# Performance work log

Measured on AMD Instinct MI355X. Metric: run time of the kernel, lower is better.

The kernel has to match this reference:

```python
import jax, jax.numpy as jnp
import numpy as np

H = 1024
NH = 16
HD = H // NH

def setup_inputs() -> dict:
    key = jax.random.key(0)
    ks = jax.random.split(key, 8)
    s = 1.0 / np.sqrt(H)
    hidden_states = jax.random.normal(ks[0], (2, 2048, H), dtype=jnp.float32)
    attention_mask = jnp.zeros((2, 1, 1, 2048), dtype=jnp.float32)
    Wq = jax.random.uniform(ks[1], (H, H), jnp.float32, -s, s)
    bq = jax.random.uniform(ks[2], (H,), jnp.float32, -s, s)
    Wk = jax.random.uniform(ks[3], (H, H), jnp.float32, -s, s)
    bk = jax.random.uniform(ks[4], (H,), jnp.float32, -s, s)
    Wv = jax.random.uniform(ks[5], (H, H), jnp.float32, -s, s)
    bv = jax.random.uniform(ks[6], (H,), jnp.float32, -s, s)
    return {"hidden_states": hidden_states, "attention_mask": attention_mask,
            "Wq": Wq, "bq": bq, "Wk": Wk, "bk": bk, "Wv": Wv, "bv": bv}

def _split_heads(x):
    B, L, _ = x.shape
    return x.reshape(B, L, NH, HD).transpose(0, 2, 1, 3)  # [B, nh, L, hd]

def reference(hidden_states, attention_mask, Wq, bq, Wk, bk, Wv, bv):
    # QKV projections (nn.Linear: x @ W.T + b)
    Q = _split_heads(hidden_states @ Wq.T + bq)
    K = _split_heads(hidden_states @ Wk.T + bk)
    V = _split_heads(hidden_states @ Wv.T + bv)
    scale = 1.0 / np.sqrt(HD)
    scores = jnp.einsum('bhqd,bhkd->bhqk', Q, K) * scale  # [B, nh, L, L]
    scores = scores + attention_mask
    probs = jax.nn.softmax(scores, axis=-1)  # dropout in eval mode = identity
    context = jnp.einsum('bhqk,bhkd->bhqd', probs, V)
    B, _, L, _ = context.shape
    return context.transpose(0, 2, 1, 3).reshape(B, L, H)
```

## Files before the change

kernel.cpp:

```cpp
#include <hip/hip_runtime.h>
#include <math.h>
#include <stdint.h>

#define H_DIM 1024
#define NH 16
#define HD 64
#define B_DIM 2
#define L_DIM 2048
#define M_TOT (B_DIM * L_DIM)

typedef __bf16 bf16_t;
typedef __bf16 bf16x8 __attribute__((ext_vector_type(8)));
typedef __bf16 bf16x4 __attribute__((ext_vector_type(4)));
typedef float  f32x4  __attribute__((ext_vector_type(4)));

#define AS1 const __attribute__((address_space(1))) void*
#define AS3 __attribute__((address_space(3))) void*

__global__ __launch_bounds__(256)
void cast_all(const float* __restrict__ x,
              const float* __restrict__ Wq, const float* __restrict__ Wk,
              const float* __restrict__ Wv, bf16_t* __restrict__ dst)
{
    const size_t idx = ((size_t)blockIdx.x * 256 + threadIdx.x) * 4;
    const float* src;
    size_t off;
    if (idx < (size_t)M_TOT * H_DIM) { src = x; off = idx; }
    else {
        size_t j = idx - (size_t)M_TOT * H_DIM;
        int z = (int)(j >> 20);
        off = j & ((1u << 20) - 1);
        src = (z == 0) ? Wq : (z == 1) ? Wk : Wv;
    }
    const float4 v = *(const float4*)(src + off);
    bf16x4 o;
    o[0] = (bf16_t)v.x; o[1] = (bf16_t)v.y;
    o[2] = (bf16_t)v.z; o[3] = (bf16_t)v.w;
    *(bf16x4*)(dst + idx) = o;
}

__global__ __launch_bounds__(256, 2)
void qkv_mfma(const bf16_t* __restrict__ xb, const bf16_t* __restrict__ wb,
              const float* __restrict__ bq, const float* __restrict__ bk,
              const float* __restrict__ bv,
              bf16_t* __restrict__ qb, bf16_t* __restrict__ kb,
              bf16_t* __restrict__ vt)
{
    __shared__ bf16_t As0[128 * 32];
    __shared__ bf16_t As1[128 * 32];
    __shared__ bf16_t As2[128 * 32];
    __shared__ bf16_t Bs0[3][64 * 32];
    __shared__ bf16_t Bs1[3][64 * 32];
    __shared__ bf16_t Bs2[3][64 * 32];

    const int tid = threadIdx.x;
    const int n   = blockIdx.x;
    const int m8  = n >> 3;
    const int bn  = ((n & 7) * 2 + (m8 & 1)) * 64;
    const int bm  = (m8 >> 1) * 128;

    const int wave = tid >> 6;
    const int lane = tid & 63;
    const int lc   = lane & 15;
    const int quad = lane >> 4;

    f32x4 acc[3][2][4];
    #pragma unroll
    for (int z = 0; z < 3; ++z)
        #pragma unroll
        for (int i = 0; i < 2; ++i)
            #pragma unroll
            for (int j = 0; j < 4; ++j)
                acc[z][i][j] = (f32x4){0.f, 0.f, 0.f, 0.f};

    const int srow = tid >> 2;
    const int sseg = tid & 3;
    const bf16_t* gA = xb + (size_t)(bm + srow) * H_DIM + (sseg ^ (srow & 3)) * 8;
    const bf16_t* gB = wb + (size_t)(bn + srow) * H_DIM + (sseg ^ (srow & 3)) * 8;
    const int woff = wave * 1024;

    auto stage = [&](int k0, bf16_t* A_, bf16_t (*B_)[64 * 32]) {
        __builtin_amdgcn_global_load_lds((AS1)(gA + k0),
            (AS3)((char*)A_ + woff), 16, 0, 0);
        __builtin_amdgcn_global_load_lds((AS1)(gA + k0 + (size_t)64 * H_DIM),
            (AS3)((char*)A_ + woff + 4096), 16, 0, 0);
        #pragma unroll
        for (int z = 0; z < 3; ++z)
            __builtin_amdgcn_global_load_lds(
                (AS1)(gB + (size_t)z * H_DIM * H_DIM + k0),
                (AS3)((char*)B_[z] + woff), 16, 0, 0);
    };

    const int slot = (quad ^ (lc & 3)) * 8;
    auto compute = [&](const bf16_t* A_, const bf16_t (*B_)[64 * 32]) {
        bf16x8 a[2];
        #pragma unroll
        for (int mi = 0; mi < 2; ++mi)
            a[mi] = *(const bf16x8*)(A_ + (wave * 32 + mi * 16 + lc) * 32 + slot);
        #pragma unroll
        for (int z = 0; z < 3; ++z) {
            bf16x8 b[4];
            #pragma unroll
            for (int ni = 0; ni < 4; ++ni)
                b[ni] = *(const bf16x8*)(B_[z] + (ni * 16 + lc) * 32 + slot);
            #pragma unroll
            for (int mi = 0; mi < 2; ++mi)
                #pragma unroll
                for (int ni = 0; ni < 4; ++ni)
                    acc[z][mi][ni] = __builtin_amdgcn_mfma_f32_16x16x32_bf16(
                        a[mi], b[ni], acc[z][mi][ni], 0, 0, 0);
        }
    };

    auto step = [&](int kk, bf16_t* cA, bf16_t (*cB)[64 * 32],
                    bf16_t* nA, bf16_t (*nB)[64 * 32], bool doStage) {
        __builtin_amdgcn_s_waitcnt(0x0F75);
        __builtin_amdgcn_s_barrier();
        if (doStage) stage((kk + 2) * 32, nA, nB);
        compute(cA, cB);
    };

    stage(0,  As0, Bs0);
    stage(32, As1, Bs1);
    #pragma unroll 1
    for (int t = 0; t < 10; ++t) {
        const int kk = t * 3;
        step(kk,     As0, Bs0, As2, Bs2, true);
        step(kk + 1, As1, Bs1, As0, Bs0, true);
        step(kk + 2, As2, Bs2, As1, Bs1, true);
    }
    step(30, As0, Bs0, As2, Bs2, false);
    __builtin_amdgcn_s_waitcnt(0x0F70);
    __builtin_amdgcn_s_barrier();
    compute(As1, Bs1);

    #pragma unroll
    for (int z = 0; z < 3; ++z) {
        const float* bias = (z == 0) ? bq : (z == 1) ? bk : bv;
        float biasv[4];
        #pragma unroll
        for (int ni = 0; ni < 4; ++ni) biasv[ni] = bias[bn + ni * 16 + lc];

        #pragma unroll
        for (int mi = 0; mi < 2; ++mi) {
            const int m0 = bm + wave * 32 + mi * 16 + quad * 4;
            if (z == 2) {
                const int b_ = m0 >> 11;
                const int l0 = m0 & 2047;
                #pragma unroll
                for (int ni = 0; ni < 4; ++ni) {
                    const int nn = bn + ni * 16 + lc;
                    const int h = nn >> 6, d = nn & 63;
                    bf16x4 pk;
                    #pragma unroll
                    for (int r = 0; r < 4; ++r)
                        pk[r] = (bf16_t)(acc[z][mi][ni][r] + biasv[ni]);
                    *(bf16x4*)(vt + (((size_t)(b_ * NH + h)) * HD + d) * L_DIM + l0) = pk;
                }
            } else {
                bf16_t* dst = (z == 0) ? qb : kb;
                #pragma unroll
                for (int r = 0; r < 4; ++r) {
                    const int m  = m0 + r;
                    const int b_ = m >> 11;
                    const int l  = m & 2047;
                    #pragma unroll
                    for (int ni = 0; ni < 4; ++ni) {
                        const int nn = bn + ni * 16 + lc;
                        const int h = nn >> 6, d = nn & 63;
                        dst[(((size_t)(b_ * NH + h)) * L_DIM + l) * HD + d] =
                            (bf16_t)(acc[z][mi][ni][r] + biasv[ni]);
                    }
                }
            }
        }
    }
}

#define EXP_C   0.180336879f
#define LOG2E   1.442695041f
#define EXP_SH  11.541560327f

__device__ __forceinline__ void attn_tile32(
    int kbase, bool pre,
    const bf16_t* curK, const bf16_t* curV,
    bf16_t* nxtK, bf16_t* nxtV,
    const bf16_t* gKw, const bf16_t* gVw, int wo,
    bf16_t* Ps, const float* mrow, int lc, int quad,
    const bf16x8 (&bQ)[2][2], f32x4 (&o)[2][4], float (&rs)[2])
{
    __builtin_amdgcn_s_waitcnt(0x0F70);
    __builtin_amdgcn_s_barrier();

    const int e = lc & 7;

    bf16x8 kf[2][2];
    #pragma unroll
    for (int ni = 0; ni < 2; ++ni) {
        const bf16_t* p = curK + (ni * 16 + lc) * 64;
        kf[ni][0] = *(const bf16x8*)(p + ((quad ^ e) << 3));
        kf[ni][1] = *(const bf16x8*)(p + (((quad ^ e) ^ 4) << 3));
    }

    if (pre) {
        const int nk = kbase + 32;
        #pragma unroll
        for (int i = 0; i < 2; ++i) {
            __builtin_amdgcn_global_load_lds(
                (AS1)(gKw + (size_t)nk * 64 + i * 512),
                (AS3)(nxtK + wo + i * 512), 16, 0, 0);
            __builtin_amdgcn_global_load_lds(
                (AS1)(gVw + nk + (size_t)i * 32768),
                (AS3)(nxtV + wo + i * 512), 16, 0, 0);
        }
    }

    float mvs[2][4];
    #pragma unroll
    for (int ni = 0; ni < 2; ++ni) {
        const float4 mv = *(const float4*)(mrow + kbase + ni * 16 + quad * 4);
        mvs[ni][0] = mv.x * LOG2E - EXP_SH;
        mvs[ni][1] = mv.y * LOG2E - EXP_SH;
        mvs[ni][2] = mv.z * LOG2E - EXP_SH;
        mvs[ni][3] = mv.w * LOG2E - EXP_SH;
    }

    #pragma unroll
    for (int f = 0; f < 2; ++f) {
        f32x4 s[2];
        #pragma unroll
        for (int ni = 0; ni < 2; ++ni) {
            f32x4 t = (f32x4){0.f, 0.f, 0.f, 0.f};
            t = __builtin_amdgcn_mfma_f32_16x16x32_bf16(kf[ni][0], bQ[f][0], t, 0, 0, 0);
            t = __builtin_amdgcn_mfma_f32_16x16x32_bf16(kf[ni][1], bQ[f][1], t, 0, 0, 0);
            s[ni] = t;
        }
        float acc = 0.f;
        #pragma unroll
        for (int ni = 0; ni < 2; ++ni) {
            bf16x4 pk;
            #pragma unroll
            for (int r = 0; r < 4; ++r) {
                const float p = __builtin_amdgcn_exp2f(s[ni][r] * EXP_C + mvs[ni][r]);
                acc += p;
                pk[r] = (bf16_t)p;
            }
            const int c = f * 4 + ni * 2 + (quad >> 1);
            *(bf16x4*)(Ps + lc * 64 + ((c ^ e) << 3) + ((quad & 1) << 2)) = pk;
        }
        rs[f] += acc;
    }

    bf16x8 vf[4];
    const int e2 = lc >> 1;
    #pragma unroll
    for (int dg = 0; dg < 4; ++dg) {
        const int p  = dg * 8 + (lc >> 1);
        const int ch = (((lc & 1) << 2) + quad) ^ e2;
        vf[dg] = *(const bf16x8*)(curV + p * 64 + (ch << 3));
    }

    #pragma unroll
    for (int f = 0; f < 2; ++f) {
        const int c = f * 4 + quad;
        const bf16x8 bP = *(const bf16x8*)(Ps + lc * 64 + ((c ^ e) << 3));
        #pragma unroll
        for (int dg = 0; dg < 4; ++dg)
            o[f][dg] = __builtin_amdgcn_mfma_f32_16x16x32_bf16(vf[dg], bP, o[f][dg], 0, 0, 0);
    }
}

__global__ __launch_bounds__(128, 4)
void attn_mfma(const bf16_t* __restrict__ qb, const bf16_t* __restrict__ kb,
               const bf16_t* __restrict__ vt, const float* __restrict__ mask,
               float* __restrict__ out, float* __restrict__ o1,
               float* __restrict__ l0, float* __restrict__ l1)
{
    __shared__ bf16_t Ks0[32 * 64];
    __shared__ bf16_t Ks1[32 * 64];
    __shared__ bf16_t Vs0[32 * 64];
    __shared__ bf16_t Vs1[32 * 64];
    __shared__ bf16_t Ps[2][16 * 64];

    const int tid  = threadIdx.x;
    const int wave = tid >> 6;
    const int lane = tid & 63;
    const int lc   = lane & 15;
    const int quad = lane >> 4;
    const int rl   = lane >> 3;
    const int sg   = lane & 7;

    const int n    = blockIdx.x;
    const int bh   = (n & 7) * 4 + ((n >> 3) & 3);
    const int q0   = ((n >> 5) & 31) * 64 + wave * 32;
    const int kh   = (n >> 10) & 1;
    const int k0   = kh << 10;
    const int b_   = bh >> 4;
    const int h    = bh & 15;

    bf16_t* Psw = Ps[wave];

    bf16x8 bQ[2][2];
    #pragma unroll
    for (int f = 0; f < 2; ++f) {
        const bf16_t* Qp = qb + ((size_t)bh * L_DIM + q0 + f * 16 + lc) * HD + quad * 8;
        bQ[f][0] = *(const bf16x8*)(Qp);
        bQ[f][1] = *(const bf16x8*)(Qp + 32);
    }

    const bf16_t* Kbase = kb + (size_t)bh * L_DIM * HD;
    const bf16_t* Vbase = vt + (size_t)bh * HD * L_DIM;
    const float*  mrow  = mask + (size_t)b_ * L_DIM + k0;

    const int cV = sg ^ rl;
    const bf16_t* gKw = Kbase + (size_t)(k0 + rl) * 64 + (sg ^ rl) * 8
                      + (size_t)wave * 1024;
    const bf16_t* gVw = Vbase + k0 + (size_t)(rl * 2 + (cV >> 2)) * L_DIM
                      + (cV & 3) * 8 + (size_t)wave * 65536;
    const int wo = wave * 1024;

    f32x4 o[2][4];
    #pragma unroll
    for (int f = 0; f < 2; ++f)
        #pragma unroll
        for (int dg = 0; dg < 4; ++dg) o[f][dg] = (f32x4){0.f, 0.f, 0.f, 0.f};
    float rs[2] = {0.f, 0.f};

    #pragma unroll
    for (int i = 0; i < 2; ++i) {
        __builtin_amdgcn_global_load_lds(
            (AS1)(gKw + i * 512),
            (AS3)(Ks0 + wo + i * 512), 16, 0, 0);
        __builtin_amdgcn_global_load_lds(
            (AS1)(gVw + (size_t)i * 32768),
            (AS3)(Vs0 + wo + i * 512), 16, 0, 0);
    }

    #pragma unroll 1
    for (int t2 = 0; t2 < 16; ++t2) {
        const int kb0 = t2 * 64;
        attn_tile32(kb0,      true,     Ks0, Vs0, Ks1, Vs1, gKw, gVw, wo, Psw,
                    mrow, lc, quad, bQ, o, rs);
        attn_tile32(kb0 + 32, t2 < 15,  Ks1, Vs1, Ks0, Vs0, gKw, gVw, wo, Psw,
                    mrow, lc, quad, bQ, o, rs);
    }

    float* obase = (kh == 0) ? out : o1;
    float* lbase = (kh == 0) ? l0  : l1;
    #pragma unroll
    for (int f = 0; f < 2; ++f) {
        float l = rs[f];
        l += __shfl_xor(l, 16);
        l += __shfl_xor(l, 32);
        if (quad == 0)
            lbase[(size_t)bh * L_DIM + q0 + f * 16 + lc] = l;
        float* orow = obase + ((size_t)(b_ * L_DIM + q0 + f * 16 + lc)) * H_DIM
                    + h * HD + quad * 4;
        #pragma unroll
        for (int dg = 0; dg < 4; ++dg)
            *(f32x4*)(orow + dg * 16) = o[f][dg];
    }
}

__global__ __launch_bounds__(256)
void attn_combine(const float* __restrict__ o1,
                  const float* __restrict__ l0, const float* __restrict__ l1,
                  float* __restrict__ out)
{
    const size_t idx = ((size_t)blockIdx.x * 256 + threadIdx.x) * 4;
    const int m   = (int)(idx >> 10);
    const int col = (int)(idx & 1023);
    const int b_  = m >> 11;
    const int q   = m & 2047;
    const int h   = col >> 6;
    const size_t lidx = ((size_t)(b_ * NH + h)) * L_DIM + q;
    const float inv = 1.0f / (l0[lidx] + l1[lidx]);
    f32x4 a = *(const f32x4*)(out + idx);
    const f32x4 b = *(const f32x4*)(o1 + idx);
    a = (a + b) * inv;
    *(f32x4*)(out + idx) = a;
}

extern "C" void kernel_launch(void* const* d_in, const int* in_sizes, int n_in,
                              void* d_out, int out_size, void* d_ws, size_t ws_size,
                              hipStream_t stream) {
    const float* hidden = (const float*)d_in[0];
    const float* mask   = (const float*)d_in[1];
    const float* Wq     = (const float*)d_in[2];
    const float* bq     = (const float*)d_in[3];
    const float* Wk     = (const float*)d_in[4];
    const float* bk     = (const float*)d_in[5];
    const float* Wv     = (const float*)d_in[6];
    const float* bv     = (const float*)d_in[7];
    float* out = (float*)d_out;

    const size_t XN = (size_t)M_TOT * H_DIM;
    const size_t WN = (size_t)3 * H_DIM * H_DIM;
    bf16_t* xwb = (bf16_t*)d_ws;
    bf16_t* qb  = xwb + XN + WN;
    bf16_t* kb  = qb + XN;
    bf16_t* vt  = kb + XN;
    float*  o1  = (float*)(vt + XN);
    float*  l0  = o1 + XN;
    float*  l1  = l0 + (size_t)B_DIM * NH * L_DIM;

    cast_all<<<(int)((XN + WN) / 1024), 256, 0, stream>>>(hidden, Wq, Wk, Wv, xwb);

    qkv_mfma<<<512, 256, 0, stream>>>(xwb, xwb + XN, bq, bk, bv, qb, kb, vt);

    attn_mfma<<<2048, 128, 0, stream>>>(qb, kb, vt, mask, out, o1, l0, l1);

    attn_combine<<<4096, 256, 0, stream>>>(o1, l0, l1, out);
}
```

Before: 179.1 us.

## Shrink QKV GEMM tile with double buffering and widen attention blocks to four waves

The QKV projection kernel moves from a 128x64 triple-buffered tile to a 64x64 double-buffered tile. Each wave now owns one 16-column slice across all three projections, the grid doubles, and the occupancy hint rises to 4 blocks per CU. The attention kernel now runs 4 waves per block over 128 queries, so each K/V tile staged in shared memory serves twice as many queries and each wave issues half the staging loads. The aim is more occupancy and more K/V reuse per shared-memory load, at the cost of less A-operand reuse in the GEMM and shallower prefetch.

```diff
diff --git a/kernel.cpp b/kernel.cpp
--- a/kernel.cpp
+++ b/kernel.cpp
@@ -39,39 +39,34 @@
     *(bf16x4*)(dst + idx) = o;
 }
 
-__global__ __launch_bounds__(256, 2)
+__global__ __launch_bounds__(256, 4)
 void qkv_mfma(const bf16_t* __restrict__ xb, const bf16_t* __restrict__ wb,
               const float* __restrict__ bq, const float* __restrict__ bk,
               const float* __restrict__ bv,
               bf16_t* __restrict__ qb, bf16_t* __restrict__ kb,
               bf16_t* __restrict__ vt)
 {
-    __shared__ bf16_t As0[128 * 32];
-    __shared__ bf16_t As1[128 * 32];
-    __shared__ bf16_t As2[128 * 32];
+    __shared__ bf16_t As0[64 * 32];
+    __shared__ bf16_t As1[64 * 32];
     __shared__ bf16_t Bs0[3][64 * 32];
     __shared__ bf16_t Bs1[3][64 * 32];
-    __shared__ bf16_t Bs2[3][64 * 32];
 
     const int tid = threadIdx.x;
     const int n   = blockIdx.x;
-    const int m8  = n >> 3;
-    const int bn  = ((n & 7) * 2 + (m8 & 1)) * 64;
-    const int bm  = (m8 >> 1) * 128;
+    const int bn  = ((n & 7) * 2 + ((n >> 3) & 1)) * 64;
+    const int bm  = (n >> 4) * 64;
 
     const int wave = tid >> 6;
     const int lane = tid & 63;
     const int lc   = lane & 15;
     const int quad = lane >> 4;
 
-    f32x4 acc[3][2][4];
+    f32x4 acc[3][4];
     #pragma unroll
     for (int z = 0; z < 3; ++z)
         #pragma unroll
-        for (int i = 0; i < 2; ++i)
-            #pragma unroll
-            for (int j = 0; j < 4; ++j)
-                acc[z][i][j] = (f32x4){0.f, 0.f, 0.f, 0.f};
+        for (int i = 0; i < 4; ++i)
+            acc[z][i] = (f32x4){0.f, 0.f, 0.f, 0.f};
 
     const int srow = tid >> 2;
     const int sseg = tid & 3;
@@ -82,8 +77,6 @@
     auto stage = [&](int k0, bf16_t* A_, bf16_t (*B_)[64 * 32]) {
         __builtin_amdgcn_global_load_lds((AS1)(gA + k0),
             (AS3)((char*)A_ + woff), 16, 0, 0);
-        __builtin_amdgcn_global_load_lds((AS1)(gA + k0 + (size_t)64 * H_DIM),
-            (AS3)((char*)A_ + woff + 4096), 16, 0, 0);
         #pragma unroll
         for (int z = 0; z < 3; ++z)
             __builtin_amdgcn_global_load_lds(
@@ -93,84 +86,66 @@
 
     const int slot = (quad ^ (lc & 3)) * 8;
     auto compute = [&](const bf16_t* A_, const bf16_t (*B_)[64 * 32]) {
-        bf16x8 a[2];
-        #pragma unroll
-        for (int mi = 0; mi < 2; ++mi)
-            a[mi] = *(const bf16x8*)(A_ + (wave * 32 + mi * 16 + lc) * 32 + slot);
-        #pragma unroll
-        for (int z = 0; z < 3; ++z) {
-            bf16x8 b[4];
+        bf16x8 b[3];
+        #pragma unroll
+        for (int z = 0; z < 3; ++z)
+            b[z] = *(const bf16x8*)(B_[z] + (wave * 16 + lc) * 32 + slot);
+        bf16x8 a[4];
+        #pragma unroll
+        for (int mi = 0; mi < 4; ++mi)
+            a[mi] = *(const bf16x8*)(A_ + (mi * 16 + lc) * 32 + slot);
+        #pragma unroll
+        for (int z = 0; z < 3; ++z)
             #pragma unroll
-            for (int ni = 0; ni < 4; ++ni)
-                b[ni] = *(const bf16x8*)(B_[z] + (ni * 16 + lc) * 32 + slot);
-            #pragma unroll
-            for (int mi = 0; mi < 2; ++mi)
-                #pragma unroll
-                for (int ni = 0; ni < 4; ++ni)
-                    acc[z][mi][ni] = __builtin_amdgcn_mfma_f32_16x16x32_bf16(
-                        a[mi], b[ni], acc[z][mi][ni], 0, 0, 0);
-        }
+            for (int mi = 0; mi < 4; ++mi)
+                acc[z][mi] = __builtin_amdgcn_mfma_f32_16x16x32_bf16(
+                    a[mi], b[z], acc[z][mi], 0, 0, 0);
     };
 
-    auto step = [&](int kk, bf16_t* cA, bf16_t (*cB)[64 * 32],
-                    bf16_t* nA, bf16_t (*nB)[64 * 32], bool doStage) {
-        __builtin_amdgcn_s_waitcnt(0x0F75);
+    stage(0, As0, Bs0);
+    #pragma unroll 1
+    for (int t = 0; t < 15; ++t) {
+        __builtin_amdgcn_s_waitcnt(0x0F70);
         __builtin_amdgcn_s_barrier();
-        if (doStage) stage((kk + 2) * 32, nA, nB);
-        compute(cA, cB);
-    };
-
-    stage(0,  As0, Bs0);
-    stage(32, As1, Bs1);
-    #pragma unroll 1
-    for (int t = 0; t < 10; ++t) {
-        const int kk = t * 3;
-        step(kk,     As0, Bs0, As2, Bs2, true);
-        step(kk + 1, As1, Bs1, As0, Bs0, true);
-        step(kk + 2, As2, Bs2, As1, Bs1, true);
-    }
-    step(30, As0, Bs0, As2, Bs2, false);
+        stage((2 * t + 1) * 32, As1, Bs1);
+        compute(As0, Bs0);
+        __builtin_amdgcn_s_waitcnt(0x0F70);
+        __builtin_amdgcn_s_barrier();
+        stage((2 * t + 2) * 32, As0, Bs0);
+        compute(As1, Bs1);
+    }
+    __builtin_amdgcn_s_waitcnt(0x0F70);
+    __builtin_amdgcn_s_barrier();
+    stage(31 * 32, As1, Bs1);
+    compute(As0, Bs0);
     __builtin_amdgcn_s_waitcnt(0x0F70);
     __builtin_amdgcn_s_barrier();
     compute(As1, Bs1);
 
+    const int col = bn + wave * 16 + lc;
+    const int h = col >> 6, d = col & 63;
     #pragma unroll
     for (int z = 0; z < 3; ++z) {
         const float* bias = (z == 0) ? bq : (z == 1) ? bk : bv;
-        float biasv[4];
-        #pragma unroll
-        for (int ni = 0; ni < 4; ++ni) biasv[ni] = bias[bn + ni * 16 + lc];
-
-        #pragma unroll
-        for (int mi = 0; mi < 2; ++mi) {
-            const int m0 = bm + wave * 32 + mi * 16 + quad * 4;
+        const float bv_ = bias[col];
+        #pragma unroll
+        for (int mi = 0; mi < 4; ++mi) {
+            const int m0 = bm + mi * 16 + quad * 4;
+            const int b_ = m0 >> 11;
             if (z == 2) {
-                const int b_ = m0 >> 11;
                 const int l0 = m0 & 2047;
+                bf16x4 pk;
                 #pragma unroll
-                for (int ni = 0; ni < 4; ++ni) {
-                    const int nn = bn + ni * 16 + lc;
-                    const int h = nn >> 6, d = nn & 63;
-                    bf16x4 pk;
-                    #pragma unroll
-                    for (int r = 0; r < 4; ++r)
-                        pk[r] = (bf16_t)(acc[z][mi][ni][r] + biasv[ni]);
-                    *(bf16x4*)(vt + (((size_t)(b_ * NH + h)) * HD + d) * L_DIM + l0) = pk;
-                }
+                for (int r = 0; r < 4; ++r)
+                    pk[r] = (bf16_t)(acc[z][mi][r] + bv_);
+                *(bf16x4*)(vt + (((size_t)(b_ * NH + h)) * HD + d) * L_DIM + l0) = pk;
             } else {
                 bf16_t* dst = (z == 0) ? qb : kb;
                 #pragma unroll
                 for (int r = 0; r < 4; ++r) {
-                    const int m  = m0 + r;
-                    const int b_ = m >> 11;
-                    const int l  = m & 2047;
-                    #pragma unroll
-                    for (int ni = 0; ni < 4; ++ni) {
-                        const int nn = bn + ni * 16 + lc;
-                        const int h = nn >> 6, d = nn & 63;
-                        dst[(((size_t)(b_ * NH + h)) * L_DIM + l) * HD + d] =
-                            (bf16_t)(acc[z][mi][ni][r] + biasv[ni]);
-                    }
+                    const int l = (m0 + r) & 2047;
+                    dst[(((size_t)(b_ * NH + h)) * L_DIM + l) * HD + d] =
+                        (bf16_t)(acc[z][mi][r] + bv_);
                 }
             }
         }
@@ -204,15 +179,12 @@
 
     if (pre) {
         const int nk = kbase + 32;
-        #pragma unroll
-        for (int i = 0; i < 2; ++i) {
-            __builtin_amdgcn_global_load_lds(
-                (AS1)(gKw + (size_t)nk * 64 + i * 512),
-                (AS3)(nxtK + wo + i * 512), 16, 0, 0);
-            __builtin_amdgcn_global_load_lds(
-                (AS1)(gVw + nk + (size_t)i * 32768),
-                (AS3)(nxtV + wo + i * 512), 16, 0, 0);
-        }
+        __builtin_amdgcn_global_load_lds(
+            (AS1)(gKw + (size_t)nk * 64),
+            (AS3)(nxtK + wo), 16, 0, 0);
+        __builtin_amdgcn_global_load_lds(
+            (AS1)(gVw + nk),
+            (AS3)(nxtV + wo), 16, 0, 0);
     }
 
     float mvs[2][4];
@@ -270,7 +242,7 @@
     }
 }
 
-__global__ __launch_bounds__(128, 4)
+__global__ __launch_bounds__(256, 4)
 void attn_mfma(const bf16_t* __restrict__ qb, const bf16_t* __restrict__ kb,
                const bf16_t* __restrict__ vt, const float* __restrict__ mask,
                float* __restrict__ out, float* __restrict__ o1,
@@ -280,7 +252,7 @@
     __shared__ bf16_t Ks1[32 * 64];
     __shared__ bf16_t Vs0[32 * 64];
     __shared__ bf16_t Vs1[32 * 64];
-    __shared__ bf16_t Ps[2][16 * 64];
+    __shared__ bf16_t Ps[4][16 * 64];
 
     const int tid  = threadIdx.x;
     const int wave = tid >> 6;
@@ -292,9 +264,9 @@
 
     const int n    = blockIdx.x;
     const int bh   = (n & 7) * 4 + ((n >> 3) & 3);
-    const int q0   = ((n >> 5) & 31) * 64 + wave * 32;
-    const int kh   = (n >> 10) & 1;
-    const int k0   = kh << 10;
+    const int q0   = ((n >> 5) & 15) * 128 + wave * 32;
+    const int ks   = (n >> 9) & 1;
+    const int k0   = ks << 10;
     const int b_   = bh >> 4;
     const int h    = bh & 15;
 
@@ -313,11 +285,11 @@
     const float*  mrow  = mask + (size_t)b_ * L_DIM + k0;
 
     const int cV = sg ^ rl;
-    const bf16_t* gKw = Kbase + (size_t)(k0 + rl) * 64 + (sg ^ rl) * 8
-                      + (size_t)wave * 1024;
-    const bf16_t* gVw = Vbase + k0 + (size_t)(rl * 2 + (cV >> 2)) * L_DIM
-                      + (cV & 3) * 8 + (size_t)wave * 65536;
-    const int wo = wave * 1024;
+    const bf16_t* gKw = Kbase + (size_t)(k0 + wave * 8 + rl) * 64 + (sg ^ rl) * 8;
+    const bf16_t* gVw = Vbase + k0
+                      + (size_t)(wave * 16 + rl * 2 + (cV >> 2)) * L_DIM
+                      + (cV & 3) * 8;
+    const int wo = wave * 512;
 
     f32x4 o[2][4];
     #pragma unroll
@@ -326,15 +298,8 @@
         for (int dg = 0; dg < 4; ++dg) o[f][dg] = (f32x4){0.f, 0.f, 0.f, 0.f};
     float rs[2] = {0.f, 0.f};
 
-    #pragma unroll
-    for (int i = 0; i < 2; ++i) {
-        __builtin_amdgcn_global_load_lds(
-            (AS1)(gKw + i * 512),
-            (AS3)(Ks0 + wo + i * 512), 16, 0, 0);
-        __builtin_amdgcn_global_load_lds(
-            (AS1)(gVw + (size_t)i * 32768),
-            (AS3)(Vs0 + wo + i * 512), 16, 0, 0);
-    }
+    __builtin_amdgcn_global_load_lds((AS1)(gKw), (AS3)(Ks0 + wo), 16, 0, 0);
+    __builtin_amdgcn_global_load_lds((AS1)(gVw), (AS3)(Vs0 + wo), 16, 0, 0);
 
     #pragma unroll 1
     for (int t2 = 0; t2 < 16; ++t2) {
@@ -345,8 +310,8 @@
                     mrow, lc, quad, bQ, o, rs);
     }
 
-    float* obase = (kh == 0) ? out : o1;
-    float* lbase = (kh == 0) ? l0  : l1;
+    float* obase = (ks == 0) ? out : o1;
+    float* lbase = (ks == 0) ? l0  : l1;
     #pragma unroll
     for (int f = 0; f < 2; ++f) {
         float l = rs[f];
@@ -406,9 +371,9 @@
 
     cast_all<<<(int)((XN + WN) / 1024), 256, 0, stream>>>(hidden, Wq, Wk, Wv, xwb);
 
-    qkv_mfma<<<512, 256, 0, stream>>>(xwb, xwb + XN, bq, bk, bv, qb, kb, vt);
-
-    attn_mfma<<<2048, 128, 0, stream>>>(qb, kb, vt, mask, out, o1, l0, l1);
+    qkv_mfma<<<1024, 256, 0, stream>>>(xwb, xwb + XN, bq, bk, bv, qb, kb, vt);
+
+    attn_mfma<<<1024, 256, 0, stream>>>(qb, kb, vt, mask, out, o1, l0, l1);
 
     attn_combine<<<4096, 256, 0, stream>>>(o1, l0, l1, out);
 }
```

After: 181.9 us. Within noise of the previous version (+1.6%).
